# Kernel optimization log

Hardware: AMD Instinct MI355X
Metric: run time of the kernel (lower is better)

Reference implementation:

```python
import jax, jax.numpy as jnp
import numpy as np

N_SEQ, N_RES, C_M = 512, 384, 256
C_O, C_Z = 32, 128  # num_outer_channel, num_output_channel
LN_EPS = 1e-5
NORM_EPS = 1e-3


def setup_inputs() -> dict:
    key = jax.random.key(0)
    ks = jax.random.split(key, 8)
    scale = 1.0 / np.sqrt(C_M)
    return {
        "act": jax.random.normal(ks[0], (N_SEQ, N_RES, C_M), dtype=jnp.float32),
        "mask": jax.random.uniform(ks[1], (N_SEQ, N_RES), dtype=jnp.float32),
        "ln_w": jnp.ones((C_M,), dtype=jnp.float32),
        "ln_b": jnp.zeros((C_M,), dtype=jnp.float32),
        "left_w": jax.random.normal(ks[2], (C_O, C_M), dtype=jnp.float32) * scale,
        "left_b": jnp.zeros((C_O,), dtype=jnp.float32),
        "right_w": jax.random.normal(ks[3], (C_O, C_M), dtype=jnp.float32) * scale,
        "right_b": jnp.zeros((C_O,), dtype=jnp.float32),
        "output_w": jax.random.normal(ks[4], (C_O, C_O, C_Z), dtype=jnp.float32) * (1.0 / C_O),
        "output_b": jnp.zeros((C_Z,), dtype=jnp.float32),
    }


def reference(act, mask, ln_w, ln_b, left_w, left_b, right_w, right_b, output_w, output_b):
    # LayerNorm over c_m
    mu = jnp.mean(act, axis=-1, keepdims=True)
    var = jnp.var(act, axis=-1, keepdims=True)
    act_n = (act - mu) * jax.lax.rsqrt(var + LN_EPS) * ln_w + ln_b

    m = mask[..., None]  # [s, r, 1]
    left = m * (jnp.einsum("src,oc->sro", act_n, left_w) + left_b)    # [s, r, co]
    right = m * (jnp.einsum("src,oc->sro", act_n, right_w) + right_b)  # [s, r, co]

    # outer product over sequence dim, then contract with output_w:
    # out[b, d, f] = sum_{a, c, e} left[a, b, c] * right[a, d, e] * w[c, e, f]
    outer = jnp.einsum("abc,ade->bdce", left, right)          # [r, r, co, co]
    out = jnp.einsum("bdce,cef->bdf", outer, output_w) + output_b  # [r, r, c_z]

    norm = jnp.einsum("sb,sd->bd", mask, mask)[..., None]  # [r, r, 1]
    return out / (NORM_EPS + norm)
```

## Files before the change

kernel.cpp:

```cpp
#include <hip/hip_runtime.h>

typedef short short8 __attribute__((ext_vector_type(8)));
typedef short short4v __attribute__((ext_vector_type(4)));
typedef float f32x4 __attribute__((ext_vector_type(4)));
typedef unsigned short ushort_t;

#define DEV_INLINE __device__ __forceinline__

constexpr int NSEQ = 512, NRES = 384, CM = 256, CO = 32, CZ = 128;
constexpr float F_LN_EPS = 1e-5f, F_NORM_EPS = 1e-3f;

constexpr size_t WS_LT   = 0;
constexpr size_t WS_RT   = WS_LT + (size_t)12288 * 512 * 2;
constexpr size_t WS_WT   = WS_RT + (size_t)12288 * 512 * 2;
constexpr size_t WS_NORM = WS_WT + (size_t)128 * 1024 * 2;
constexpr size_t WS_PW   = WS_NORM + (size_t)384 * 384 * 4;

DEV_INLINE ushort_t f2bf(float x) {
  union { float f; unsigned u; } v; v.f = x;
  unsigned r = v.u + 0x7FFFu + ((v.u >> 16) & 1u);
  return (ushort_t)(r >> 16);
}

DEV_INLINE short8 pack8(float4 a, float4 b) {
  short8 p;
  p[0] = (short)f2bf(a.x); p[1] = (short)f2bf(a.y);
  p[2] = (short)f2bf(a.z); p[3] = (short)f2bf(a.w);
  p[4] = (short)f2bf(b.x); p[5] = (short)f2bf(b.y);
  p[6] = (short)f2bf(b.z); p[7] = (short)f2bf(b.w);
  return p;
}

DEV_INLINE void async16(const void* g, void* l) {
  __builtin_amdgcn_global_load_lds(
      (const __attribute__((address_space(1))) unsigned*)g,
      (__attribute__((address_space(3))) unsigned*)l, 16, 0, 0);
}

__global__ __launch_bounds__(256) void k_wt(const float* __restrict__ W,
                                            ushort_t* __restrict__ WT2) {
  int tid = blockIdx.x * 256 + threadIdx.x;
  int k = tid >> 7, f = tid & 127;
  WT2[((size_t)(k >> 3) * 128 + f) * 8 + (k & 7)] = f2bf(W[(size_t)k * CZ + f]);
}

__global__ __launch_bounds__(256) void k_pack(const float* __restrict__ left_w,
                                              const float* __restrict__ right_w,
                                              ushort_t* __restrict__ PW) {
  int id = blockIdx.x * 256 + threadIdx.x;
  int o = id >> 5, ch = id & 31;
  const float* src = (o < 32 ? left_w + (size_t)o * CM
                             : right_w + (size_t)(o - 32) * CM) + ch * 8;
  float4 a = *(const float4*)src, b = *(const float4*)(src + 4);
  *(short8*)&PW[(size_t)o * CM + ch * 8] = pack8(a, b);
}

__global__ __launch_bounds__(256) void k_norm(const float* __restrict__ mask,
                                              float* __restrict__ normM) {
  int b = blockIdx.x * 16 + threadIdx.x;
  int d = blockIdx.y * 16 + threadIdx.y;
  float a0 = 0.f, a1 = 0.f, a2 = 0.f, a3 = 0.f;
  for (int a = 0; a < NSEQ; a += 4) {
    a0 += mask[(size_t)(a + 0) * NRES + b] * mask[(size_t)(a + 0) * NRES + d];
    a1 += mask[(size_t)(a + 1) * NRES + b] * mask[(size_t)(a + 1) * NRES + d];
    a2 += mask[(size_t)(a + 2) * NRES + b] * mask[(size_t)(a + 2) * NRES + d];
    a3 += mask[(size_t)(a + 3) * NRES + b] * mask[(size_t)(a + 3) * NRES + d];
  }
  normM[(size_t)b * NRES + d] = (a0 + a1) + (a2 + a3);
}

__global__ __launch_bounds__(256) void k_lnproj(
    const float* __restrict__ act, const float* __restrict__ mask,
    const float* __restrict__ ln_w, const float* __restrict__ ln_b,
    const float* __restrict__ left_b, const float* __restrict__ right_b,
    const ushort_t* __restrict__ PW,
    ushort_t* __restrict__ Lt, ushort_t* __restrict__ Rt) {
  __shared__ ushort_t sAct[16 * 256];

  const int t = threadIdx.x;
  const int a0 = blockIdx.x * 16;
  const int b = blockIdx.y;
  const int r = t >> 4, c = t & 15;

  const float4* arow =
      (const float4*)(act + ((size_t)(a0 + r) * NRES + b) * CM + c * 16);
  float4 v[4];
  float s = 0.f, ss = 0.f;
#pragma unroll
  for (int j = 0; j < 4; j++) {
    v[j] = arow[j];
    s += v[j].x + v[j].y + v[j].z + v[j].w;
    ss += v[j].x * v[j].x + v[j].y * v[j].y + v[j].z * v[j].z + v[j].w * v[j].w;
  }
  s += __shfl_xor(s, 1);  s += __shfl_xor(s, 2);
  s += __shfl_xor(s, 4);  s += __shfl_xor(s, 8);
  ss += __shfl_xor(ss, 1); ss += __shfl_xor(ss, 2);
  ss += __shfl_xor(ss, 4); ss += __shfl_xor(ss, 8);
  const float mu = s * (1.f / CM);
  const float rs = rsqrtf(ss * (1.f / CM) - mu * mu + F_LN_EPS);

  const int lane = t & 63, w = t >> 6;
  const int q = lane >> 4, ln = lane & 15;
  short8 bfrag[8];
#pragma unroll
  for (int ks = 0; ks < 8; ks++)
    bfrag[ks] = *(const short8*)&PW[(size_t)(w * 16 + ln) * CM + (ks * 4 + q) * 8];

#pragma unroll
  for (int j = 0; j < 2; j++) {
    int cb = c * 16 + j * 8;
    float4 lw0 = *(const float4*)(ln_w + cb), lw1 = *(const float4*)(ln_w + cb + 4);
    float4 lb0 = *(const float4*)(ln_b + cb), lb1 = *(const float4*)(ln_b + cb + 4);
    float4 x0 = v[2 * j], x1 = v[2 * j + 1], y0, y1;
    y0.x = (x0.x - mu) * rs * lw0.x + lb0.x;
    y0.y = (x0.y - mu) * rs * lw0.y + lb0.y;
    y0.z = (x0.z - mu) * rs * lw0.z + lb0.z;
    y0.w = (x0.w - mu) * rs * lw0.w + lb0.w;
    y1.x = (x1.x - mu) * rs * lw1.x + lb1.x;
    y1.y = (x1.y - mu) * rs * lw1.y + lb1.y;
    y1.z = (x1.z - mu) * rs * lw1.z + lb1.z;
    y1.w = (x1.w - mu) * rs * lw1.w + lb1.w;
    int chunk = c * 2 + j;
    *(short8*)&sAct[r * 256 + ((chunk ^ (r & 7)) * 8)] = pack8(y0, y1);
  }
  __syncthreads();

  f32x4 acc = {0, 0, 0, 0};
#pragma unroll
  for (int ks = 0; ks < 8; ks++) {
    int kc = ks * 4 + q;
    short8 af = *(const short8*)&sAct[ln * 256 + ((kc ^ (ln & 7)) * 8)];
    acc = __builtin_amdgcn_mfma_f32_16x16x32_bf16(af, bfrag[ks], acc, 0, 0, 0);
  }

  const int o = w * 16 + ln;
  float mk[4];
#pragma unroll
  for (int reg = 0; reg < 4; reg++)
    mk[reg] = mask[(size_t)(a0 + q * 4 + reg) * NRES + b];
  float bias = (o < 32) ? left_b[o] : right_b[o - 32];
  ushort_t* dst = (o < 32) ? (Lt + (size_t)(b * 32 + o) * NSEQ)
                           : (Rt + (size_t)(b * 32 + (o - 32)) * NSEQ);
  short4v pk;
#pragma unroll
  for (int reg = 0; reg < 4; reg++)
    pk[reg] = (short)f2bf((acc[reg] + bias) * mk[reg]);
  *(short4v*)&dst[a0 + q * 4] = pk;
}

__global__ __launch_bounds__(256, 2) void k_opm(
    const ushort_t* __restrict__ Lt, const ushort_t* __restrict__ Rt,
    const ushort_t* __restrict__ WT2, const float* __restrict__ normM,
    const float* __restrict__ out_b, float* __restrict__ out) {
  __shared__ ushort_t smem[32768];
  ushort_t* sP = smem;

  const int t = threadIdx.x, lane = t & 63, w = t >> 6;
  const int q = lane >> 4, ln = lane & 15;
  const int wm = w & 1, wn = w >> 1;
  const int m0 = blockIdx.x * 128, n0 = blockIdx.y * 128;
  const int srow8 = lane >> 3, schunk = lane & 7;

  auto STAGE = [&](int kt, int c) {
    ushort_t* base = smem + c * 16384;
#pragma unroll
    for (int i = 0; i < 4; i++) {
      int rg = w + i * 4;
      int r = rg * 8 + srow8;
      int gc = schunk ^ (r & 7);
      async16(Lt + (size_t)(m0 + r) * NSEQ + kt * 64 + gc * 8, (char*)base + rg * 1024);
      async16(Rt + (size_t)(n0 + r) * NSEQ + kt * 64 + gc * 8,
              (char*)base + 16384 + rg * 1024);
    }
  };

  f32x4 acc1[4][4];
#pragma unroll
  for (int i = 0; i < 4; i++)
#pragma unroll
    for (int j = 0; j < 4; j++) acc1[i][j] = {0, 0, 0, 0};

  STAGE(0, 0);
  asm volatile("s_waitcnt vmcnt(0)" ::: "memory");
  __builtin_amdgcn_s_barrier();
#pragma unroll
  for (int kt = 0; kt < 8; kt++) {
    const int cur = kt & 1;
    if (kt + 1 < 8) STAGE(kt + 1, cur ^ 1);

    const ushort_t* bA = smem + cur * 16384;
    const ushort_t* bB = bA + 8192;
#pragma unroll
    for (int ks = 0; ks < 2; ks++) {
      int kc = ks * 4 + q;
      short8 af[4], bf[4];
#pragma unroll
      for (int tm = 0; tm < 4; tm++) {
        int rr = wm * 64 + tm * 16 + ln;
        af[tm] = *(const short8*)&bA[rr * 64 + ((kc ^ (rr & 7)) * 8)];
      }
#pragma unroll
      for (int tn = 0; tn < 4; tn++) {
        int rr = wn * 64 + tn * 16 + ln;
        bf[tn] = *(const short8*)&bB[rr * 64 + ((kc ^ (rr & 7)) * 8)];
      }
      __builtin_amdgcn_s_setprio(1);
#pragma unroll
      for (int tm = 0; tm < 4; tm++)
#pragma unroll
        for (int tn = 0; tn < 4; tn++)
          acc1[tm][tn] =
              __builtin_amdgcn_mfma_f32_16x16x32_bf16(af[tm], bf[tn], acc1[tm][tn], 0, 0, 0);
      __builtin_amdgcn_s_setprio(0);
    }
    asm volatile("s_waitcnt vmcnt(0)" ::: "memory");
    __builtin_amdgcn_s_barrier();
  }

  __syncthreads();
#pragma unroll
  for (int tm = 0; tm < 4; tm++) {
#pragma unroll
    for (int tn = 0; tn < 4; tn++) {
      int pair = (wm * 2 + (tm >> 1)) * 4 + (wn * 2 + (tn >> 1));
      int e = (tn & 1) * 16 + ln;
#pragma unroll
      for (int reg = 0; reg < 4; reg++) {
        int c = (tm & 1) * 16 + q * 4 + reg;
        int ce = c * 32 + e;
        int pos = (ce >> 3) ^ (pair & 7);
        sP[pair * 1024 + pos * 8 + (ce & 7)] = f2bf(acc1[tm][tn][reg]);
      }
    }
  }
  __syncthreads();

  f32x4 acc2[2] = {{0, 0, 0, 0}, {0, 0, 0, 0}};
#pragma unroll
  for (int kt = 0; kt < 16; kt++) {
#pragma unroll
    for (int ks = 0; ks < 2; ks++) {
      int c16 = kt * 8 + ks * 4 + q;
      short8 af = *(const short8*)&sP[ln * 1024 + ((c16 ^ (ln & 7)) * 8)];
#pragma unroll
      for (int tn = 0; tn < 2; tn++) {
        int fr = w * 32 + tn * 16 + ln;
        short8 bfr = *(const short8*)&WT2[((size_t)c16 * 128 + fr) * 8];
        acc2[tn] = __builtin_amdgcn_mfma_f32_16x16x32_bf16(af, bfr, acc2[tn], 0, 0, 0);
      }
    }
  }

  const int b = blockIdx.x * 4 + q;
#pragma unroll
  for (int reg = 0; reg < 4; reg++) {
    int d = blockIdx.y * 4 + reg;
    float inv = 1.f / (F_NORM_EPS + normM[(size_t)b * NRES + d]);
#pragma unroll
    for (int tn = 0; tn < 2; tn++) {
      int f = w * 32 + tn * 16 + ln;
      out[((size_t)b * NRES + d) * CZ + f] = (acc2[tn][reg] + out_b[f]) * inv;
    }
  }
}

extern "C" void kernel_launch(void* const* d_in, const int* in_sizes, int n_in,
                              void* d_out, int out_size, void* d_ws, size_t ws_size,
                              hipStream_t stream) {
  (void)in_sizes; (void)n_in; (void)out_size; (void)ws_size;
  const float* act      = (const float*)d_in[0];
  const float* mask     = (const float*)d_in[1];
  const float* ln_w     = (const float*)d_in[2];
  const float* ln_b     = (const float*)d_in[3];
  const float* left_w   = (const float*)d_in[4];
  const float* left_b   = (const float*)d_in[5];
  const float* right_w  = (const float*)d_in[6];
  const float* right_b  = (const float*)d_in[7];
  const float* output_w = (const float*)d_in[8];
  const float* output_b = (const float*)d_in[9];
  float* out = (float*)d_out;

  char* ws = (char*)d_ws;
  ushort_t* Lt = (ushort_t*)(ws + WS_LT);
  ushort_t* Rt = (ushort_t*)(ws + WS_RT);
  ushort_t* WT2 = (ushort_t*)(ws + WS_WT);
  float* normM = (float*)(ws + WS_NORM);
  ushort_t* PW = (ushort_t*)(ws + WS_PW);

  hipLaunchKernelGGL(k_pack, dim3(8), dim3(256), 0, stream, left_w, right_w, PW);
  hipLaunchKernelGGL(k_wt, dim3(512), dim3(256), 0, stream, output_w, WT2);
  hipLaunchKernelGGL(k_norm, dim3(24, 24), dim3(16, 16), 0, stream, mask, normM);
  hipLaunchKernelGGL(k_lnproj, dim3(32, 384), dim3(256), 0, stream, act, mask,
                     ln_w, ln_b, left_b, right_b, PW, Lt, Rt);
  hipLaunchKernelGGL(k_opm, dim3(96, 96), dim3(256), 0, stream, Lt, Rt, WT2,
                     normM, output_b, out);
}
```

Before: 590.6 us.

## Pre-swizzle left operand into MFMA fragment layout and load it directly to registers

The projection kernel now writes the left operand in a tiled layout that matches the MFMA A-fragment order, so the outer-product kernel reads A fragments straight from global memory into double-buffered registers instead of staging them through LDS. Only the right operand still goes through LDS, which halves the shared memory per block and could raise occupancy. The block index mapping is also swapped so blockIdx.x walks the right/column tiles, which changes which blocks share L2 data. The cost is more registers held for A fragments, and the A loads become per-lane global reads whose latency must be hidden behind the MFMA work.

```diff
diff --git a/kernel.cpp b/kernel.cpp
--- a/kernel.cpp
+++ b/kernel.cpp
@@ -74,7 +74,7 @@
     const float* __restrict__ ln_w, const float* __restrict__ ln_b,
     const float* __restrict__ left_b, const float* __restrict__ right_b,
     const ushort_t* __restrict__ PW,
-    ushort_t* __restrict__ Lt, ushort_t* __restrict__ Rt) {
+    ushort_t* __restrict__ Lt2, ushort_t* __restrict__ Rt) {
   __shared__ ushort_t sAct[16 * 256];
 
   const int t = threadIdx.x;
@@ -139,66 +139,81 @@
   for (int reg = 0; reg < 4; reg++)
     mk[reg] = mask[(size_t)(a0 + q * 4 + reg) * NRES + b];
   float bias = (o < 32) ? left_b[o] : right_b[o - 32];
-  ushort_t* dst = (o < 32) ? (Lt + (size_t)(b * 32 + o) * NSEQ)
-                           : (Rt + (size_t)(b * 32 + (o - 32)) * NSEQ);
   short4v pk;
 #pragma unroll
   for (int reg = 0; reg < 4; reg++)
     pk[reg] = (short)f2bf((acc[reg] + bias) * mk[reg]);
-  *(short4v*)&dst[a0 + q * 4] = pk;
+
+  const int a = a0 + q * 4;
+  if (o < 32) {
+    int rr = b * 32 + o;
+    *(short4v*)&Lt2[((size_t)(rr >> 4) * 64 + (a >> 3)) * 128 + (rr & 15) * 8 + (a & 7)] = pk;
+  } else {
+    *(short4v*)&Rt[(size_t)(b * 32 + (o - 32)) * NSEQ + a] = pk;
+  }
 }
 
 __global__ __launch_bounds__(256, 2) void k_opm(
-    const ushort_t* __restrict__ Lt, const ushort_t* __restrict__ Rt,
+    const ushort_t* __restrict__ Lt2, const ushort_t* __restrict__ Rt,
     const ushort_t* __restrict__ WT2, const float* __restrict__ normM,
     const float* __restrict__ out_b, float* __restrict__ out) {
-  __shared__ ushort_t smem[32768];
+  __shared__ ushort_t smem[16384];
   ushort_t* sP = smem;
 
   const int t = threadIdx.x, lane = t & 63, w = t >> 6;
   const int q = lane >> 4, ln = lane & 15;
   const int wm = w & 1, wn = w >> 1;
-  const int m0 = blockIdx.x * 128, n0 = blockIdx.y * 128;
+  const int mby = blockIdx.y, nbx = blockIdx.x;
+  const int m0 = mby * 128, n0 = nbx * 128;
   const int srow8 = lane >> 3, schunk = lane & 7;
 
-  auto STAGE = [&](int kt, int c) {
-    ushort_t* base = smem + c * 16384;
+  auto STAGE_B = [&](int kt, int c) {
+    char* base = (char*)smem + c * 16384;
 #pragma unroll
     for (int i = 0; i < 4; i++) {
       int rg = w + i * 4;
       int r = rg * 8 + srow8;
       int gc = schunk ^ (r & 7);
-      async16(Lt + (size_t)(m0 + r) * NSEQ + kt * 64 + gc * 8, (char*)base + rg * 1024);
-      async16(Rt + (size_t)(n0 + r) * NSEQ + kt * 64 + gc * 8,
-              (char*)base + 16384 + rg * 1024);
+      async16(Rt + (size_t)(n0 + r) * NSEQ + kt * 64 + gc * 8, base + rg * 1024);
     }
   };
 
+  auto LOAD_A = [&](int kt, short8 dst[2][4]) {
+#pragma unroll
+    for (int ks = 0; ks < 2; ks++) {
+      int c32 = kt * 8 + ks * 4 + q;
+#pragma unroll
+      for (int tm = 0; tm < 4; tm++) {
+        size_t idx = ((size_t)(mby * 8 + wm * 4 + tm) * 64 + c32) * 128 + ln * 8;
+        dst[ks][tm] = *(const short8*)&Lt2[idx];
+      }
+    }
+  };
+
   f32x4 acc1[4][4];
 #pragma unroll
   for (int i = 0; i < 4; i++)
 #pragma unroll
     for (int j = 0; j < 4; j++) acc1[i][j] = {0, 0, 0, 0};
 
-  STAGE(0, 0);
+  short8 afb[2][2][4];
+
+  STAGE_B(0, 0);
+  LOAD_A(0, afb[0]);
   asm volatile("s_waitcnt vmcnt(0)" ::: "memory");
   __builtin_amdgcn_s_barrier();
 #pragma unroll
   for (int kt = 0; kt < 8; kt++) {
     const int cur = kt & 1;
-    if (kt + 1 < 8) STAGE(kt + 1, cur ^ 1);
-
-    const ushort_t* bA = smem + cur * 16384;
-    const ushort_t* bB = bA + 8192;
+    if (kt + 1 < 8) {
+      STAGE_B(kt + 1, cur ^ 1);
+      LOAD_A(kt + 1, afb[cur ^ 1]);
+    }
+    const ushort_t* bB = smem + cur * 8192;
 #pragma unroll
     for (int ks = 0; ks < 2; ks++) {
       int kc = ks * 4 + q;
-      short8 af[4], bf[4];
-#pragma unroll
-      for (int tm = 0; tm < 4; tm++) {
-        int rr = wm * 64 + tm * 16 + ln;
-        af[tm] = *(const short8*)&bA[rr * 64 + ((kc ^ (rr & 7)) * 8)];
-      }
+      short8 bf[4];
 #pragma unroll
       for (int tn = 0; tn < 4; tn++) {
         int rr = wn * 64 + tn * 16 + ln;
@@ -209,8 +224,8 @@
       for (int tm = 0; tm < 4; tm++)
 #pragma unroll
         for (int tn = 0; tn < 4; tn++)
-          acc1[tm][tn] =
-              __builtin_amdgcn_mfma_f32_16x16x32_bf16(af[tm], bf[tn], acc1[tm][tn], 0, 0, 0);
+          acc1[tm][tn] = __builtin_amdgcn_mfma_f32_16x16x32_bf16(
+              afb[cur][ks][tm], bf[tn], acc1[tm][tn], 0, 0, 0);
       __builtin_amdgcn_s_setprio(0);
     }
     asm volatile("s_waitcnt vmcnt(0)" ::: "memory");
@@ -251,10 +266,10 @@
     }
   }
 
-  const int b = blockIdx.x * 4 + q;
+  const int b = mby * 4 + q;
 #pragma unroll
   for (int reg = 0; reg < 4; reg++) {
-    int d = blockIdx.y * 4 + reg;
+    int d = nbx * 4 + reg;
     float inv = 1.f / (F_NORM_EPS + normM[(size_t)b * NRES + d]);
 #pragma unroll
     for (int tn = 0; tn < 2; tn++) {
@@ -281,17 +296,17 @@
   float* out = (float*)d_out;
 
   char* ws = (char*)d_ws;
-  ushort_t* Lt = (ushort_t*)(ws + WS_LT);
-  ushort_t* Rt = (ushort_t*)(ws + WS_RT);
+  ushort_t* Lt2 = (ushort_t*)(ws + WS_LT);
+  ushort_t* Rt  = (ushort_t*)(ws + WS_RT);
   ushort_t* WT2 = (ushort_t*)(ws + WS_WT);
-  float* normM = (float*)(ws + WS_NORM);
-  ushort_t* PW = (ushort_t*)(ws + WS_PW);
+  float* normM  = (float*)(ws + WS_NORM);
+  ushort_t* PW  = (ushort_t*)(ws + WS_PW);
 
   hipLaunchKernelGGL(k_pack, dim3(8), dim3(256), 0, stream, left_w, right_w, PW);
   hipLaunchKernelGGL(k_wt, dim3(512), dim3(256), 0, stream, output_w, WT2);
   hipLaunchKernelGGL(k_norm, dim3(24, 24), dim3(16, 16), 0, stream, mask, normM);
   hipLaunchKernelGGL(k_lnproj, dim3(32, 384), dim3(256), 0, stream, act, mask,
-                     ln_w, ln_b, left_b, right_b, PW, Lt, Rt);
-  hipLaunchKernelGGL(k_opm, dim3(96, 96), dim3(256), 0, stream, Lt, Rt, WT2,
+                     ln_w, ln_b, left_b, right_b, PW, Lt2, Rt);
+  hipLaunchKernelGGL(k_opm, dim3(96, 96), dim3(256), 0, stream, Lt2, Rt, WT2,
                      normM, output_b, out);
 }
```

New measurement: 604.0 us. 1.02x slower.

## Enlarge outer-product tile to 256x256 with 512-thread blocks and WT2 reuse

Applied to the files above, without the earlier changes.

The main outer-product kernel now gives each block a 256x256 (residue*channel) tile using 8 waves instead of 128x128 with 4 waves. Each block covers 8x8 residue pairs, which halves global loads of Lt/Rt per output and lets each WT2 fragment be reused across 4 pair tiles in the second GEMM. The cost is 128KB of LDS and 128 accumulator registers per thread, which can reduce occupancy or cause spills. The weight transpose kernel also writes packed 8-element vectors instead of single scattered shorts.

```diff
diff --git a/kernel.cpp b/kernel.cpp
--- a/kernel.cpp
+++ b/kernel.cpp
@@ -40,8 +40,12 @@
 __global__ __launch_bounds__(256) void k_wt(const float* __restrict__ W,
                                             ushort_t* __restrict__ WT2) {
   int tid = blockIdx.x * 256 + threadIdx.x;
-  int k = tid >> 7, f = tid & 127;
-  WT2[((size_t)(k >> 3) * 128 + f) * 8 + (k & 7)] = f2bf(W[(size_t)k * CZ + f]);
+  int kc = tid >> 7, f = tid & 127;
+  short8 p;
+#pragma unroll
+  for (int e = 0; e < 8; e++)
+    p[e] = (short)f2bf(W[(size_t)(kc * 8 + e) * CZ + f]);
+  *(short8*)&WT2[((size_t)kc * 128 + f) * 8] = p;
 }
 
 __global__ __launch_bounds__(256) void k_pack(const float* __restrict__ left_w,
@@ -148,35 +152,34 @@
   *(short4v*)&dst[a0 + q * 4] = pk;
 }
 
-__global__ __launch_bounds__(256, 2) void k_opm(
+__global__ __launch_bounds__(512, 2) void k_opm(
     const ushort_t* __restrict__ Lt, const ushort_t* __restrict__ Rt,
     const ushort_t* __restrict__ WT2, const float* __restrict__ normM,
     const float* __restrict__ out_b, float* __restrict__ out) {
-  __shared__ ushort_t smem[32768];
+  __shared__ ushort_t smem[65536];
   ushort_t* sP = smem;
 
   const int t = threadIdx.x, lane = t & 63, w = t >> 6;
   const int q = lane >> 4, ln = lane & 15;
-  const int wm = w & 1, wn = w >> 1;
-  const int m0 = blockIdx.x * 128, n0 = blockIdx.y * 128;
-  const int srow8 = lane >> 3, schunk = lane & 7;
+  const int wm = w >> 2, wn = w & 3;
+  const int m0 = blockIdx.x * 256, n0 = blockIdx.y * 256;
 
   auto STAGE = [&](int kt, int c) {
-    ushort_t* base = smem + c * 16384;
-#pragma unroll
-    for (int i = 0; i < 4; i++) {
-      int rg = w + i * 4;
-      int r = rg * 8 + srow8;
-      int gc = schunk ^ (r & 7);
-      async16(Lt + (size_t)(m0 + r) * NSEQ + kt * 64 + gc * 8, (char*)base + rg * 1024);
+    ushort_t* base = smem + c * 32768;
+#pragma unroll
+    for (int j = 0; j < 4; j++) {
+      int r = j * 64 + (t >> 3);
+      int gc = (t & 7) ^ (r & 7);
+      async16(Lt + (size_t)(m0 + r) * NSEQ + kt * 64 + gc * 8,
+              base + j * 4096 + t * 8);
       async16(Rt + (size_t)(n0 + r) * NSEQ + kt * 64 + gc * 8,
-              (char*)base + 16384 + rg * 1024);
+              base + 16384 + j * 4096 + t * 8);
     }
   };
 
-  f32x4 acc1[4][4];
-#pragma unroll
-  for (int i = 0; i < 4; i++)
+  f32x4 acc1[8][4];
+#pragma unroll
+  for (int i = 0; i < 8; i++)
 #pragma unroll
     for (int j = 0; j < 4; j++) acc1[i][j] = {0, 0, 0, 0};
 
@@ -188,15 +191,15 @@
     const int cur = kt & 1;
     if (kt + 1 < 8) STAGE(kt + 1, cur ^ 1);
 
-    const ushort_t* bA = smem + cur * 16384;
-    const ushort_t* bB = bA + 8192;
+    const ushort_t* bA = smem + cur * 32768;
+    const ushort_t* bB = bA + 16384;
 #pragma unroll
     for (int ks = 0; ks < 2; ks++) {
       int kc = ks * 4 + q;
-      short8 af[4], bf[4];
-#pragma unroll
-      for (int tm = 0; tm < 4; tm++) {
-        int rr = wm * 64 + tm * 16 + ln;
+      short8 af[8], bf[4];
+#pragma unroll
+      for (int tm = 0; tm < 8; tm++) {
+        int rr = wm * 128 + tm * 16 + ln;
         af[tm] = *(const short8*)&bA[rr * 64 + ((kc ^ (rr & 7)) * 8)];
       }
 #pragma unroll
@@ -206,11 +209,11 @@
       }
       __builtin_amdgcn_s_setprio(1);
 #pragma unroll
-      for (int tm = 0; tm < 4; tm++)
+      for (int tm = 0; tm < 8; tm++)
 #pragma unroll
         for (int tn = 0; tn < 4; tn++)
-          acc1[tm][tn] =
-              __builtin_amdgcn_mfma_f32_16x16x32_bf16(af[tm], bf[tn], acc1[tm][tn], 0, 0, 0);
+          acc1[tm][tn] = __builtin_amdgcn_mfma_f32_16x16x32_bf16(
+              af[tm], bf[tn], acc1[tm][tn], 0, 0, 0);
       __builtin_amdgcn_s_setprio(0);
     }
     asm volatile("s_waitcnt vmcnt(0)" ::: "memory");
@@ -219,15 +222,15 @@
 
   __syncthreads();
 #pragma unroll
-  for (int tm = 0; tm < 4; tm++) {
+  for (int tm = 0; tm < 8; tm++) {
 #pragma unroll
     for (int tn = 0; tn < 4; tn++) {
-      int pair = (wm * 2 + (tm >> 1)) * 4 + (wn * 2 + (tn >> 1));
-      int e = (tn & 1) * 16 + ln;
 #pragma unroll
       for (int reg = 0; reg < 4; reg++) {
-        int c = (tm & 1) * 16 + q * 4 + reg;
-        int ce = c * 32 + e;
+        int mabs = wm * 128 + tm * 16 + q * 4 + reg;
+        int nabs = wn * 64 + tn * 16 + ln;
+        int pair = (mabs >> 5) * 8 + (nabs >> 5);
+        int ce = (mabs & 31) * 32 + (nabs & 31);
         int pos = (ce >> 3) ^ (pair & 7);
         sP[pair * 1024 + pos * 8 + (ce & 7)] = f2bf(acc1[tm][tn][reg]);
       }
@@ -235,31 +238,33 @@
   }
   __syncthreads();
 
-  f32x4 acc2[2] = {{0, 0, 0, 0}, {0, 0, 0, 0}};
+  f32x4 acc2[4] = {{0, 0, 0, 0}, {0, 0, 0, 0}, {0, 0, 0, 0}, {0, 0, 0, 0}};
 #pragma unroll
   for (int kt = 0; kt < 16; kt++) {
 #pragma unroll
     for (int ks = 0; ks < 2; ks++) {
       int c16 = kt * 8 + ks * 4 + q;
-      short8 af = *(const short8*)&sP[ln * 1024 + ((c16 ^ (ln & 7)) * 8)];
-#pragma unroll
-      for (int tn = 0; tn < 2; tn++) {
-        int fr = w * 32 + tn * 16 + ln;
-        short8 bfr = *(const short8*)&WT2[((size_t)c16 * 128 + fr) * 8];
-        acc2[tn] = __builtin_amdgcn_mfma_f32_16x16x32_bf16(af, bfr, acc2[tn], 0, 0, 0);
+      short8 bfr = *(const short8*)&WT2[((size_t)c16 * 128 + w * 16 + ln) * 8];
+#pragma unroll
+      for (int tm2 = 0; tm2 < 4; tm2++) {
+        int p = tm2 * 16 + ln;
+        short8 af = *(const short8*)&sP[p * 1024 + ((c16 ^ (p & 7)) * 8)];
+        acc2[tm2] = __builtin_amdgcn_mfma_f32_16x16x32_bf16(af, bfr, acc2[tm2], 0, 0, 0);
       }
     }
   }
 
-  const int b = blockIdx.x * 4 + q;
-#pragma unroll
-  for (int reg = 0; reg < 4; reg++) {
-    int d = blockIdx.y * 4 + reg;
-    float inv = 1.f / (F_NORM_EPS + normM[(size_t)b * NRES + d]);
-#pragma unroll
-    for (int tn = 0; tn < 2; tn++) {
-      int f = w * 32 + tn * 16 + ln;
-      out[((size_t)b * NRES + d) * CZ + f] = (acc2[tn][reg] + out_b[f]) * inv;
+  const int f = w * 16 + ln;
+  const float ob = out_b[f];
+#pragma unroll
+  for (int tm2 = 0; tm2 < 4; tm2++) {
+#pragma unroll
+    for (int reg = 0; reg < 4; reg++) {
+      int p = tm2 * 16 + q * 4 + reg;
+      int b = blockIdx.x * 8 + (p >> 3);
+      int d = blockIdx.y * 8 + (p & 7);
+      float inv = 1.f / (F_NORM_EPS + normM[(size_t)b * NRES + d]);
+      out[((size_t)b * NRES + d) * CZ + f] = (acc2[tm2][reg] + ob) * inv;
     }
   }
 }
@@ -281,17 +286,17 @@
   float* out = (float*)d_out;
 
   char* ws = (char*)d_ws;
-  ushort_t* Lt = (ushort_t*)(ws + WS_LT);
-  ushort_t* Rt = (ushort_t*)(ws + WS_RT);
+  ushort_t* Lt  = (ushort_t*)(ws + WS_LT);
+  ushort_t* Rt  = (ushort_t*)(ws + WS_RT);
   ushort_t* WT2 = (ushort_t*)(ws + WS_WT);
-  float* normM = (float*)(ws + WS_NORM);
-  ushort_t* PW = (ushort_t*)(ws + WS_PW);
+  float* normM  = (float*)(ws + WS_NORM);
+  ushort_t* PW  = (ushort_t*)(ws + WS_PW);
 
   hipLaunchKernelGGL(k_pack, dim3(8), dim3(256), 0, stream, left_w, right_w, PW);
-  hipLaunchKernelGGL(k_wt, dim3(512), dim3(256), 0, stream, output_w, WT2);
+  hipLaunchKernelGGL(k_wt, dim3(64), dim3(256), 0, stream, output_w, WT2);
   hipLaunchKernelGGL(k_norm, dim3(24, 24), dim3(16, 16), 0, stream, mask, normM);
   hipLaunchKernelGGL(k_lnproj, dim3(32, 384), dim3(256), 0, stream, act, mask,
                      ln_w, ln_b, left_b, right_b, PW, Lt, Rt);
-  hipLaunchKernelGGL(k_opm, dim3(96, 96), dim3(256), 0, stream, Lt, Rt, WT2,
+  hipLaunchKernelGGL(k_opm, dim3(48, 48), dim3(512), 0, stream, Lt, Rt, WT2,
                      normM, output_b, out);
 }
```

Result: faster. 559.2 us (-5.3%).
